# Kernel optimization log

Hardware: AMD Instinct MI355X
Metric: run time of the kernel (lower is better)

Reference implementation:

```python
import jax, jax.numpy as jnp
import numpy as np

SCALING = 2.0  # lora_alpha / r


def setup_inputs() -> dict:
    key = jax.random.key(0)
    ks = jax.random.split(key, 6)
    B, S, D_IN, D_OUT, R = 4, 4096, 4096, 4096, 32
    x = jax.random.normal(ks[0], (B, S, D_IN), dtype=jnp.float32)
    W = jax.random.normal(ks[1], (D_OUT, D_IN), dtype=jnp.float32) * 0.02
    b = jax.random.normal(ks[2], (D_OUT,), dtype=jnp.float32) * 0.02
    A = jax.random.normal(ks[3], (R, D_IN), dtype=jnp.float32) * 0.02
    B_w = jax.random.normal(ks[4], (D_OUT, R), dtype=jnp.float32) * 0.02
    # per-sample activation offsets, in [1, S]
    alora_offsets = jax.random.randint(ks[5], (B,), 1, S + 1, dtype=jnp.int32)
    return {"x": x, "alora_offsets": alora_offsets, "W": W, "b": b, "A": A, "B_w": B_w}


def reference(x, alora_offsets, W, b, A, B_w):
    # base linear: y = x @ W^T + b
    base = jnp.einsum("bsd,od->bso", x, W) + b  # [B, S, D_OUT]
    # LoRA path on full sequence (dropout is identity at inference, p=0)
    lora = jnp.einsum("bsr,or->bso", jnp.einsum("bsd,rd->bsr", x, A), B_w) * SCALING
    # per-sample tail mask: only last k = min(offset, S) positions get the LoRA update
    S = x.shape[1]
    k = jnp.minimum(alora_offsets, S)  # [B]
    pos = jnp.arange(S, dtype=jnp.int32)
    mask = pos[None, :] >= (S - k)[:, None]  # [B, S] True on the tail
    return base + jnp.where(mask[:, :, None], lora, jnp.zeros((), base.dtype))
```

## Files before the change

kernel.cpp:

```cpp
#include <hip/hip_runtime.h>
#include <hip/hip_bf16.h>

typedef __attribute__((ext_vector_type(8))) short short8;
typedef __attribute__((ext_vector_type(4))) float f32x4;

#define GLOAD_LDS16(gp, lp)                                                      \
  __builtin_amdgcn_global_load_lds(                                              \
      (const __attribute__((address_space(1))) void*)(gp),                       \
      (__attribute__((address_space(3))) void*)(lp), 16, 0, 0)

#define SBAR() asm volatile("s_barrier" ::: "memory")
#define VMC(n)                                                                   \
  do {                                                                           \
    asm volatile("s_waitcnt vmcnt(" #n ")" ::: "memory");                        \
    __builtin_amdgcn_sched_barrier(0);                                           \
  } while (0)

__device__ __forceinline__ unsigned short f2bf_rne(float f) {
  union { float f; unsigned int u; } v; v.f = f;
  unsigned int u = v.u;
  u += 0x7fffu + ((u >> 16) & 1u);
  return (unsigned short)(u >> 16);
}

__global__ void cvt_f32_bf16(const float* __restrict__ src,
                             unsigned short* __restrict__ dst, int n8) {
  int i = blockIdx.x * blockDim.x + threadIdx.x;
  int stride = gridDim.x * blockDim.x;
  const f32x4* s4 = (const f32x4*)src;
  short8* d8 = (short8*)dst;
  for (; i < n8; i += stride) {
    f32x4 a = s4[2 * i], b = s4[2 * i + 1];
    short8 o;
    o[0] = (short)f2bf_rne(a[0]); o[1] = (short)f2bf_rne(a[1]);
    o[2] = (short)f2bf_rne(a[2]); o[3] = (short)f2bf_rne(a[3]);
    o[4] = (short)f2bf_rne(b[0]); o[5] = (short)f2bf_rne(b[1]);
    o[6] = (short)f2bf_rne(b[2]); o[7] = (short)f2bf_rne(b[3]);
    d8[i] = o;
  }
}

__global__ __launch_bounds__(256) void lora_t_kernel(
    const unsigned short* __restrict__ xb,
    const unsigned short* __restrict__ Ab,
    const int* __restrict__ offs,
    unsigned short* __restrict__ T)
{
  __shared__ unsigned short xs[64 * 64];
  __shared__ unsigned short as_[32 * 64];
  const int t = threadIdx.x;
  const int m0 = blockIdx.x * 64;
  const int l = t & 63, w = t >> 6;
  const int lr = l & 15, lk = (l >> 4) * 8;
  const int arow = t >> 3, acol = (t & 7) * 8;
  f32x4 acc0 = {0, 0, 0, 0}, acc1 = {0, 0, 0, 0};
  for (int kt = 0; kt < 64; ++kt) {
    __syncthreads();
    const int kof = kt * 64 + acol;
    GLOAD_LDS16(xb + (size_t)(m0 + arow) * 4096 + kof,      (char*)xs + (arow * 64 + acol) * 2);
    GLOAD_LDS16(xb + (size_t)(m0 + 32 + arow) * 4096 + kof, (char*)xs + ((32 + arow) * 64 + acol) * 2);
    GLOAD_LDS16(Ab + (size_t)arow * 4096 + kof,             (char*)as_ + (arow * 64 + acol) * 2);
    __syncthreads();
#pragma unroll
    for (int kk = 0; kk < 2; ++kk) {
      short8 a  = *(const short8*)&xs[(w * 16 + lr) * 64 + kk * 32 + lk];
      short8 b0 = *(const short8*)&as_[lr * 64 + kk * 32 + lk];
      short8 b1 = *(const short8*)&as_[(16 + lr) * 64 + kk * 32 + lk];
      acc0 = __builtin_amdgcn_mfma_f32_16x16x32_bf16(a, b0, acc0, 0, 0, 0);
      acc1 = __builtin_amdgcn_mfma_f32_16x16x32_bf16(a, b1, acc1, 0, 0, 0);
    }
  }
  const int rowb = (l >> 4) * 4;
#pragma unroll
  for (int j = 0; j < 4; ++j) {
    int m = m0 + w * 16 + rowb + j;
    int bb = m >> 12, s = m & 4095;
    int kcut = offs[bb]; if (kcut > 4096) kcut = 4096;
    bool keep = s >= 4096 - kcut;
    T[(size_t)m * 32 + lr]      = keep ? f2bf_rne(2.0f * acc0[j]) : (unsigned short)0;
    T[(size_t)m * 32 + 16 + lr] = keep ? f2bf_rne(2.0f * acc1[j]) : (unsigned short)0;
  }
}

__global__ __launch_bounds__(512, 2) void gemm_kernel(
    const unsigned short* __restrict__ xb,
    const unsigned short* __restrict__ Wb,
    const unsigned short* __restrict__ Tm,
    const unsigned short* __restrict__ Bwb,
    const float* __restrict__ bias,
    float* __restrict__ out)
{
  constexpr int K = 4096;
  extern __shared__ char smem[];

  const int bid = blockIdx.x;
  const int swz = (bid & 7) * 128 + (bid >> 3);
  const int m0 = (swz >> 4) * 256;
  const int n0 = (swz & 15) * 256;

  const int t = threadIdx.x;
  const int l = t & 63, w = t >> 6;
  const int wqr = w >> 2;
  const int pr = (w >> 1) & 1;
  const int pc = w & 1;
  const int lr = l & 15, hi = l >> 4;
  const int e0 = (hi ^ (lr & 7)) * 8;

  const int srow = t >> 3;
  const int schunk = ((t & 7) ^ ((t >> 3) & 7)) * 8;
  const unsigned short* pA0 = xb + (size_t)(m0 + srow) * K + schunk;
  const unsigned short* pA1 = xb + (size_t)(m0 + 128 + srow) * K + schunk;
  const unsigned short* pB0 = Wb + (size_t)(n0 + srow) * K + schunk;
  const unsigned short* pB1 = Wb + (size_t)(n0 + 128 + srow) * K + schunk;
  unsigned short* sm = (unsigned short*)smem;
  const int ldst = t * 16;

#define STG(PTR, SLOT, ISB, HALF, KT)                                           \
  do {                                                                          \
    const unsigned short* g_ = (PTR) + (KT) * 64;                               \
    char* d_ = smem + (SLOT) * 65536 + (ISB) * 32768 + (HALF) * 16384 + ldst;   \
    GLOAD_LDS16(g_, d_);                                                        \
    GLOAD_LDS16(g_ + (size_t)64 * K, d_ + 8192);                                \
  } while (0)

  f32x4 acc[2][4][4];
  short8 afr[4];

  {
    const unsigned short* tp = Tm + (size_t)(m0 + wqr * 128 + pr * 64 + lr) * 32 + hi * 8;
    short8 la[4];
#pragma unroll
    for (int i = 0; i < 4; ++i) la[i] = *(const short8*)(tp + i * 512);
    short8 lb[2][4];
#pragma unroll
    for (int qc = 0; qc < 2; ++qc)
#pragma unroll
      for (int j = 0; j < 4; ++j)
        lb[qc][j] = *(const short8*)(Bwb + (size_t)(n0 + qc * 128 + pc * 64 + j * 16 + lr) * 32 + hi * 8);
#pragma unroll
    for (int qc = 0; qc < 2; ++qc)
#pragma unroll
      for (int i = 0; i < 4; ++i)
#pragma unroll
        for (int j = 0; j < 4; ++j)
          acc[qc][i][j] = __builtin_amdgcn_mfma_f32_16x16x32_bf16(
              la[i], lb[qc][j], (f32x4){0.f, 0.f, 0.f, 0.f}, 0, 0, 0);
  }

  STG(pA0, 0, 0, 0, 0);
  STG(pA1, 0, 0, 1, 0);
  STG(pB0, 0, 1, 0, 0);
  STG(pB1, 0, 1, 1, 0);
  STG(pB0, 1, 1, 0, 1);
  VMC(2);
  SBAR();

#define PHASE(SLOT, QC, KK, READA, STG_STMT, WAIT_STMT)                         \
  {                                                                             \
    const unsigned short* Ah = sm + (SLOT) * 32768 + wqr * 8192;                \
    const unsigned short* Bh = sm + (SLOT) * 32768 + 16384 + (QC) * 8192;       \
    const int ek = e0 ^ ((KK) * 32);                                            \
    if (READA) {                                                                \
      _Pragma("unroll")                                                         \
      for (int i = 0; i < 4; ++i)                                               \
        afr[i] = *(const short8*)(Ah + (pr * 64 + i * 16 + lr) * 64 + ek);      \
    }                                                                           \
    short8 bfr[4];                                                              \
    _Pragma("unroll")                                                           \
    for (int j = 0; j < 4; ++j)                                                 \
      bfr[j] = *(const short8*)(Bh + (pc * 64 + j * 16 + lr) * 64 + ek);        \
    STG_STMT;                                                                   \
    SBAR();                                                                     \
    __builtin_amdgcn_s_setprio(1);                                              \
    _Pragma("unroll")                                                           \
    for (int i = 0; i < 4; ++i)                                                 \
      _Pragma("unroll")                                                         \
      for (int j = 0; j < 4; ++j)                                               \
        acc[QC][i][j] = __builtin_amdgcn_mfma_f32_16x16x32_bf16(                \
            afr[i], bfr[j], acc[QC][i][j], 0, 0, 0);                            \
    __builtin_amdgcn_s_setprio(0);                                              \
    WAIT_STMT;                                                                  \
    SBAR();                                                                     \
  }

  for (int I = 0; I < 31; ++I) {
    const int a = 2 * I;
    PHASE(0, 0, 0, 1, STG(pA0, 1, 0, 0, a + 1), VMC(4));
    PHASE(0, 1, 0, 0, STG(pA1, 1, 0, 1, a + 1), VMC(4));
    PHASE(0, 0, 1, 1, STG(pB1, 1, 1, 1, a + 1), VMC(4));
    PHASE(0, 1, 1, 0, STG(pB0, 0, 1, 0, a + 2), VMC(4));
    PHASE(1, 0, 0, 1, STG(pA0, 0, 0, 0, a + 2), VMC(4));
    PHASE(1, 1, 0, 0, STG(pA1, 0, 0, 1, a + 2), VMC(4));
    PHASE(1, 0, 1, 1, STG(pB1, 0, 1, 1, a + 2), VMC(4));
    PHASE(1, 1, 1, 0, STG(pB0, 1, 1, 0, a + 3), VMC(4));
  }
  PHASE(0, 0, 0, 1, STG(pA0, 1, 0, 0, 63), VMC(4));
  PHASE(0, 1, 0, 0, STG(pA1, 1, 0, 1, 63), VMC(4));
  PHASE(0, 0, 1, 1, STG(pB1, 1, 1, 1, 63), VMC(4));
  PHASE(0, 1, 1, 0, ((void)0), VMC(2));
  PHASE(1, 0, 0, 1, ((void)0), VMC(0));
  PHASE(1, 1, 0, 0, ((void)0), ((void)0));
  PHASE(1, 0, 1, 1, ((void)0), ((void)0));
  PHASE(1, 1, 1, 0, ((void)0), ((void)0));
#undef PHASE
#undef STG

  float bv[2][4];
#pragma unroll
  for (int qc = 0; qc < 2; ++qc)
#pragma unroll
    for (int j = 0; j < 4; ++j)
      bv[qc][j] = bias[n0 + qc * 128 + pc * 64 + j * 16 + lr];
  const int rowb = hi * 4;
#pragma unroll
  for (int qc = 0; qc < 2; ++qc)
#pragma unroll
    for (int i = 0; i < 4; ++i)
#pragma unroll
      for (int e = 0; e < 4; ++e) {
        int row = m0 + wqr * 128 + pr * 64 + i * 16 + rowb + e;
        float* orow = out + (size_t)row * 4096 + n0 + qc * 128 + pc * 64;
#pragma unroll
        for (int j = 0; j < 4; ++j) orow[j * 16 + lr] = acc[qc][i][j][e] + bv[qc][j];
      }
}

extern "C" void kernel_launch(void* const* d_in, const int* in_sizes, int n_in,
                              void* d_out, int out_size, void* d_ws, size_t ws_size,
                              hipStream_t stream) {
  const float* x   = (const float*)d_in[0];
  const int* offs  = (const int*)d_in[1];
  const float* W   = (const float*)d_in[2];
  const float* b   = (const float*)d_in[3];
  const float* A   = (const float*)d_in[4];
  const float* Bw  = (const float*)d_in[5];
  float* out = (float*)d_out;

  char* ws = (char*)d_ws;
  unsigned short* xb  = (unsigned short*)ws;
  unsigned short* Wb  = (unsigned short*)(ws + 134217728);
  unsigned short* Ab  = (unsigned short*)(ws + 167772160);
  unsigned short* Bwb = (unsigned short*)(ws + 168034304);
  unsigned short* T   = (unsigned short*)(ws + 168296448);

  hipFuncSetAttribute((const void*)gemm_kernel,
                      hipFuncAttributeMaxDynamicSharedMemorySize, 131072);

  cvt_f32_bf16<<<2048, 256, 0, stream>>>(x, xb, 67108864 / 8);
  cvt_f32_bf16<<<2048, 256, 0, stream>>>(W, Wb, 16777216 / 8);
  cvt_f32_bf16<<<64, 256, 0, stream>>>(A, Ab, 131072 / 8);
  cvt_f32_bf16<<<64, 256, 0, stream>>>(Bw, Bwb, 131072 / 8);
  lora_t_kernel<<<256, 256, 0, stream>>>(xb, Ab, offs, T);
  gemm_kernel<<<1024, 512, 131072, stream>>>(xb, Wb, T, Bwb, b, out);
}
```

Baseline: 604.4 us.

## Restructure main GEMM loop into windows with early-issued LDS fragment reads

Replaces the per-phase macro with a four-phase window that preloads A and B fragments for upcoming phases ahead of the barriers. The MFMA order is reshuffled (qc0/kk0, qc1/kk0, qc0/kk1, qc1/kk1) so LDS reads for the next phase can overlap the current MFMA block. The vmcnt waits in the last phase of each window are relaxed. This uses more fragment registers, which may raise VGPR pressure, and the changed wait counts must still cover the LDS slot reuse hazards.

Result: no change. 608.4 us (+0.7%).

```diff
diff --git a/kernel.cpp b/kernel.cpp
--- a/kernel.cpp
+++ b/kernel.cpp
@@ -124,7 +124,25 @@
   } while (0)
 
   f32x4 acc[2][4][4];
-  short8 afr[4];
+  short8 a0f[4], a1f[4], b0f[4], b1f[4];
+
+#define RD_A(DST, AH, KK)                                                       \
+  _Pragma("unroll")                                                             \
+  for (int i_ = 0; i_ < 4; ++i_)                                                \
+    DST[i_] = *(const short8*)((AH) + (pr * 64 + i_ * 16 + lr) * 64 + (e0 ^ ((KK) * 32)));
+
+#define RD_B(DST, BH, KK)                                                       \
+  _Pragma("unroll")                                                             \
+  for (int j_ = 0; j_ < 4; ++j_)                                                \
+    DST[j_] = *(const short8*)((BH) + (pc * 64 + j_ * 16 + lr) * 64 + (e0 ^ ((KK) * 32)));
+
+#define MFMA16(QC, AF, BF)                                                      \
+  _Pragma("unroll")                                                             \
+  for (int i_ = 0; i_ < 4; ++i_)                                                \
+    _Pragma("unroll")                                                           \
+    for (int j_ = 0; j_ < 4; ++j_)                                              \
+      acc[QC][i_][j_] = __builtin_amdgcn_mfma_f32_16x16x32_bf16(                \
+          (AF)[i_], (BF)[j_], acc[QC][i_][j_], 0, 0, 0);
 
   {
     const unsigned short* tp = Tm + (size_t)(m0 + wqr * 128 + pr * 64 + lr) * 32 + hi * 8;
@@ -155,54 +173,51 @@
   VMC(2);
   SBAR();
 
-#define PHASE(SLOT, QC, KK, READA, STG_STMT, WAIT_STMT)                         \
+#define WINDOW(SLOT, S0, S1, S2, S3, W0, W1, W2, W3)                            \
   {                                                                             \
-    const unsigned short* Ah = sm + (SLOT) * 32768 + wqr * 8192;                \
-    const unsigned short* Bh = sm + (SLOT) * 32768 + 16384 + (QC) * 8192;       \
-    const int ek = e0 ^ ((KK) * 32);                                            \
-    if (READA) {                                                                \
-      _Pragma("unroll")                                                         \
-      for (int i = 0; i < 4; ++i)                                               \
-        afr[i] = *(const short8*)(Ah + (pr * 64 + i * 16 + lr) * 64 + ek);      \
-    }                                                                           \
-    short8 bfr[4];                                                              \
-    _Pragma("unroll")                                                           \
-    for (int j = 0; j < 4; ++j)                                                 \
-      bfr[j] = *(const short8*)(Bh + (pc * 64 + j * 16 + lr) * 64 + ek);        \
-    STG_STMT;                                                                   \
-    SBAR();                                                                     \
-    __builtin_amdgcn_s_setprio(1);                                              \
-    _Pragma("unroll")                                                           \
-    for (int i = 0; i < 4; ++i)                                                 \
-      _Pragma("unroll")                                                         \
-      for (int j = 0; j < 4; ++j)                                               \
-        acc[QC][i][j] = __builtin_amdgcn_mfma_f32_16x16x32_bf16(                \
-            afr[i], bfr[j], acc[QC][i][j], 0, 0, 0);                            \
-    __builtin_amdgcn_s_setprio(0);                                              \
-    WAIT_STMT;                                                                  \
-    SBAR();                                                                     \
+    const unsigned short* Ah  = sm + (SLOT) * 32768 + wqr * 8192;               \
+    const unsigned short* B0h = sm + (SLOT) * 32768 + 16384;                    \
+    const unsigned short* B1h = sm + (SLOT) * 32768 + 16384 + 8192;             \
+    RD_A(a0f, Ah, 0); RD_B(b0f, B0h, 0);                \
+                                                             \
+    RD_B(b1f, B1h, 0);                                                          \
+    S0; SBAR();                                                                 \
+    __builtin_amdgcn_s_setprio(1); MFMA16(0, a0f, b0f);                         \
+    __builtin_amdgcn_s_setprio(0); W0; SBAR();                                  \
+                                                             \
+    RD_A(a1f, Ah, 1); RD_B(b0f, B0h, 1);                                        \
+    S1; SBAR();                                                                 \
+    __builtin_amdgcn_s_setprio(1); MFMA16(1, a0f, b1f);                         \
+    __builtin_amdgcn_s_setprio(0); W1; SBAR();                                  \
+                                                             \
+    RD_B(b1f, B1h, 1);                                                          \
+    S2; SBAR();                                                                 \
+    __builtin_amdgcn_s_setprio(1); MFMA16(0, a1f, b0f);                         \
+    __builtin_amdgcn_s_setprio(0); W2; SBAR();                                  \
+                                                             \
+    S3; SBAR();                                                                 \
+    __builtin_amdgcn_s_setprio(1); MFMA16(1, a1f, b1f);                         \
+    __builtin_amdgcn_s_setprio(0); W3; SBAR();                                  \
   }
 
   for (int I = 0; I < 31; ++I) {
     const int a = 2 * I;
-    PHASE(0, 0, 0, 1, STG(pA0, 1, 0, 0, a + 1), VMC(4));
-    PHASE(0, 1, 0, 0, STG(pA1, 1, 0, 1, a + 1), VMC(4));
-    PHASE(0, 0, 1, 1, STG(pB1, 1, 1, 1, a + 1), VMC(4));
-    PHASE(0, 1, 1, 0, STG(pB0, 0, 1, 0, a + 2), VMC(4));
-    PHASE(1, 0, 0, 1, STG(pA0, 0, 0, 0, a + 2), VMC(4));
-    PHASE(1, 1, 0, 0, STG(pA1, 0, 0, 1, a + 2), VMC(4));
-    PHASE(1, 0, 1, 1, STG(pB1, 0, 1, 1, a + 2), VMC(4));
-    PHASE(1, 1, 1, 0, STG(pB0, 1, 1, 0, a + 3), VMC(4));
-  }
-  PHASE(0, 0, 0, 1, STG(pA0, 1, 0, 0, 63), VMC(4));
-  PHASE(0, 1, 0, 0, STG(pA1, 1, 0, 1, 63), VMC(4));
-  PHASE(0, 0, 1, 1, STG(pB1, 1, 1, 1, 63), VMC(4));
-  PHASE(0, 1, 1, 0, ((void)0), VMC(2));
-  PHASE(1, 0, 0, 1, ((void)0), VMC(0));
-  PHASE(1, 1, 0, 0, ((void)0), ((void)0));
-  PHASE(1, 0, 1, 1, ((void)0), ((void)0));
-  PHASE(1, 1, 1, 0, ((void)0), ((void)0));
-#undef PHASE
+    WINDOW(0, STG(pA0, 1, 0, 0, a + 1), STG(pA1, 1, 0, 1, a + 1),
+              STG(pB1, 1, 1, 1, a + 1), STG(pB0, 0, 1, 0, a + 2),
+              VMC(4), VMC(4), VMC(4), VMC(2));
+    WINDOW(1, STG(pA0, 0, 0, 0, a + 2), STG(pA1, 0, 0, 1, a + 2),
+              STG(pB1, 0, 1, 1, a + 2), STG(pB0, 1, 1, 0, a + 3),
+              VMC(4), VMC(4), VMC(4), VMC(2));
+  }
+  WINDOW(0, STG(pA0, 1, 0, 0, 63), STG(pA1, 1, 0, 1, 63),
+            STG(pB1, 1, 1, 1, 63), ((void)0),
+            VMC(4), VMC(4), VMC(2), VMC(0));
+  WINDOW(1, ((void)0), ((void)0), ((void)0), ((void)0),
+            ((void)0), ((void)0), ((void)0), ((void)0));
+#undef WINDOW
+#undef MFMA16
+#undef RD_A
+#undef RD_B
 #undef STG
 
   float bv[2][4];
```

## Switch main GEMM to 32x32x16 MFMA with reworked LDS pipeline schedule

Applied to the files above, without the earlier changes.

Replaces the 16x16x32 bf16 MFMA tiling with 32x32x16 MFMA, so each wave computes 2x2x2 tiles of 32x32 and uses fewer LDS reads per FLOP. The pipeline is restructured too: each K-slot now has four k-sub-phases that each load full A and B fragments, staging is grouped as whole-A and whole-B double-buffer loads, and waits are a full vmcnt(0) once per slot instead of fine-grained vmcnt(4). The LoRA init and epilogue are adapted to the 32x32 accumulator layout. The coarser waits may expose more load latency.

New measurement: 662.7 us. +9.6%, slower.

```diff
diff --git a/kernel.cpp b/kernel.cpp
--- a/kernel.cpp
+++ b/kernel.cpp
@@ -3,6 +3,7 @@
 
 typedef __attribute__((ext_vector_type(8))) short short8;
 typedef __attribute__((ext_vector_type(4))) float f32x4;
+typedef __attribute__((ext_vector_type(16))) float f32x16;
 
 #define GLOAD_LDS16(gp, lp)                                                      \
   __builtin_amdgcn_global_load_lds(                                              \
@@ -103,8 +104,8 @@
   const int wqr = w >> 2;
   const int pr = (w >> 1) & 1;
   const int pc = w & 1;
-  const int lr = l & 15, hi = l >> 4;
-  const int e0 = (hi ^ (lr & 7)) * 8;
+  const int la = l & 31, ksel = l >> 5;
+  const int cxor = la & 7;
 
   const int srow = t >> 3;
   const int schunk = ((t & 7) ^ ((t >> 3) & 7)) * 8;
@@ -122,107 +123,110 @@
     GLOAD_LDS16(g_, d_);                                                        \
     GLOAD_LDS16(g_ + (size_t)64 * K, d_ + 8192);                                \
   } while (0)
-
-  f32x4 acc[2][4][4];
-  short8 afr[4];
+#define STGA(SLOT, KT) do { STG(pA0, SLOT, 0, 0, KT); STG(pA1, SLOT, 0, 1, KT); } while (0)
+#define STGB(SLOT, KT) do { STG(pB0, SLOT, 1, 0, KT); STG(pB1, SLOT, 1, 1, KT); } while (0)
+
+  const int rowbase = m0 + wqr * 128 + pr * 64;
+  const int arowbase = (wqr * 128 + pr * 64) * 64;
+
+  f32x16 acc[2][2][2];
 
   {
-    const unsigned short* tp = Tm + (size_t)(m0 + wqr * 128 + pr * 64 + lr) * 32 + hi * 8;
-    short8 la[4];
-#pragma unroll
-    for (int i = 0; i < 4; ++i) la[i] = *(const short8*)(tp + i * 512);
-    short8 lb[2][4];
+    short8 ta[2][2];
+#pragma unroll
+    for (int i = 0; i < 2; ++i)
+#pragma unroll
+      for (int ks = 0; ks < 2; ++ks)
+        ta[i][ks] = *(const short8*)(Tm + (size_t)(rowbase + i * 32 + la) * 32 + ks * 16 + ksel * 8);
+    const f32x16 z16 = {0.f, 0.f, 0.f, 0.f, 0.f, 0.f, 0.f, 0.f,
+                        0.f, 0.f, 0.f, 0.f, 0.f, 0.f, 0.f, 0.f};
 #pragma unroll
     for (int qc = 0; qc < 2; ++qc)
 #pragma unroll
-      for (int j = 0; j < 4; ++j)
-        lb[qc][j] = *(const short8*)(Bwb + (size_t)(n0 + qc * 128 + pc * 64 + j * 16 + lr) * 32 + hi * 8);
-#pragma unroll
-    for (int qc = 0; qc < 2; ++qc)
-#pragma unroll
-      for (int i = 0; i < 4; ++i)
-#pragma unroll
-        for (int j = 0; j < 4; ++j)
-          acc[qc][i][j] = __builtin_amdgcn_mfma_f32_16x16x32_bf16(
-              la[i], lb[qc][j], (f32x4){0.f, 0.f, 0.f, 0.f}, 0, 0, 0);
-  }
-
-  STG(pA0, 0, 0, 0, 0);
-  STG(pA1, 0, 0, 1, 0);
-  STG(pB0, 0, 1, 0, 0);
-  STG(pB1, 0, 1, 1, 0);
-  STG(pB0, 1, 1, 0, 1);
-  VMC(2);
+      for (int j = 0; j < 2; ++j) {
+        const unsigned short* bp = Bwb + (size_t)(n0 + qc * 128 + pc * 64 + j * 32 + la) * 32;
+        short8 tb0 = *(const short8*)(bp + ksel * 8);
+        short8 tb1 = *(const short8*)(bp + 16 + ksel * 8);
+#pragma unroll
+        for (int i = 0; i < 2; ++i) {
+          f32x16 v = __builtin_amdgcn_mfma_f32_32x32x16_bf16(ta[i][0], tb0, z16, 0, 0, 0);
+          acc[qc][i][j] = __builtin_amdgcn_mfma_f32_32x32x16_bf16(ta[i][1], tb1, v, 0, 0, 0);
+        }
+      }
+  }
+
+  STGA(0, 0); STGB(0, 0);
+  VMC(0);
   SBAR();
 
-#define PHASE(SLOT, QC, KK, READA, STG_STMT, WAIT_STMT)                         \
+#define PHASE(SLOT, KS, WAIT, ...)                                              \
   {                                                                             \
-    const unsigned short* Ah = sm + (SLOT) * 32768 + wqr * 8192;                \
-    const unsigned short* Bh = sm + (SLOT) * 32768 + 16384 + (QC) * 8192;       \
-    const int ek = e0 ^ ((KK) * 32);                                            \
-    if (READA) {                                                                \
+    const unsigned short* Sb = sm + (SLOT) * 32768;                             \
+    const int ck = ((((KS) * 2) + ksel) ^ cxor) * 8;                            \
+    short8 afr[2], bfr[2][2];                                                   \
+    _Pragma("unroll")                                                           \
+    for (int i_ = 0; i_ < 2; ++i_)                                              \
+      afr[i_] = *(const short8*)(Sb + arowbase + (i_ * 32 + la) * 64 + ck);     \
+    _Pragma("unroll")                                                           \
+    for (int q_ = 0; q_ < 2; ++q_)                                              \
       _Pragma("unroll")                                                         \
-      for (int i = 0; i < 4; ++i)                                               \
-        afr[i] = *(const short8*)(Ah + (pr * 64 + i * 16 + lr) * 64 + ek);      \
-    }                                                                           \
-    short8 bfr[4];                                                              \
-    _Pragma("unroll")                                                           \
-    for (int j = 0; j < 4; ++j)                                                 \
-      bfr[j] = *(const short8*)(Bh + (pc * 64 + j * 16 + lr) * 64 + ek);        \
-    STG_STMT;                                                                   \
+      for (int j_ = 0; j_ < 2; ++j_)                                            \
+        bfr[q_][j_] = *(const short8*)(Sb + 16384 +                             \
+            (q_ * 128 + pc * 64 + j_ * 32 + la) * 64 + ck);                     \
+    __VA_ARGS__;                                                                \
     SBAR();                                                                     \
     __builtin_amdgcn_s_setprio(1);                                              \
     _Pragma("unroll")                                                           \
-    for (int i = 0; i < 4; ++i)                                                 \
+    for (int q_ = 0; q_ < 2; ++q_)                                              \
       _Pragma("unroll")                                                         \
-      for (int j = 0; j < 4; ++j)                                               \
-        acc[QC][i][j] = __builtin_amdgcn_mfma_f32_16x16x32_bf16(                \
-            afr[i], bfr[j], acc[QC][i][j], 0, 0, 0);                            \
+      for (int i_ = 0; i_ < 2; ++i_)                                            \
+        _Pragma("unroll")                                                       \
+        for (int j_ = 0; j_ < 2; ++j_)                                          \
+          acc[q_][i_][j_] = __builtin_amdgcn_mfma_f32_32x32x16_bf16(            \
+              afr[i_], bfr[q_][j_], acc[q_][i_][j_], 0, 0, 0);                  \
     __builtin_amdgcn_s_setprio(0);                                              \
-    WAIT_STMT;                                                                  \
+    WAIT;                                                                       \
     SBAR();                                                                     \
   }
 
   for (int I = 0; I < 31; ++I) {
     const int a = 2 * I;
-    PHASE(0, 0, 0, 1, STG(pA0, 1, 0, 0, a + 1), VMC(4));
-    PHASE(0, 1, 0, 0, STG(pA1, 1, 0, 1, a + 1), VMC(4));
-    PHASE(0, 0, 1, 1, STG(pB1, 1, 1, 1, a + 1), VMC(4));
-    PHASE(0, 1, 1, 0, STG(pB0, 0, 1, 0, a + 2), VMC(4));
-    PHASE(1, 0, 0, 1, STG(pA0, 0, 0, 0, a + 2), VMC(4));
-    PHASE(1, 1, 0, 0, STG(pA1, 0, 0, 1, a + 2), VMC(4));
-    PHASE(1, 0, 1, 1, STG(pB1, 0, 1, 1, a + 2), VMC(4));
-    PHASE(1, 1, 1, 0, STG(pB0, 1, 1, 0, a + 3), VMC(4));
-  }
-  PHASE(0, 0, 0, 1, STG(pA0, 1, 0, 0, 63), VMC(4));
-  PHASE(0, 1, 0, 0, STG(pA1, 1, 0, 1, 63), VMC(4));
-  PHASE(0, 0, 1, 1, STG(pB1, 1, 1, 1, 63), VMC(4));
-  PHASE(0, 1, 1, 0, ((void)0), VMC(2));
-  PHASE(1, 0, 0, 1, ((void)0), VMC(0));
-  PHASE(1, 1, 0, 0, ((void)0), ((void)0));
-  PHASE(1, 0, 1, 1, ((void)0), ((void)0));
-  PHASE(1, 1, 1, 0, ((void)0), ((void)0));
+    PHASE(0, 0, ((void)0), STGA(1, a + 1));
+    PHASE(0, 1, ((void)0), STGB(1, a + 1));
+    PHASE(0, 2, ((void)0), );
+    PHASE(0, 3, VMC(0), );
+    PHASE(1, 0, ((void)0), STGA(0, a + 2));
+    PHASE(1, 1, ((void)0), STGB(0, a + 2));
+    PHASE(1, 2, ((void)0), );
+    PHASE(1, 3, VMC(0), );
+  }
+  PHASE(0, 0, ((void)0), STGA(1, 63));
+  PHASE(0, 1, ((void)0), STGB(1, 63));
+  PHASE(0, 2, ((void)0), );
+  PHASE(0, 3, VMC(0), );
+  PHASE(1, 0, ((void)0), );
+  PHASE(1, 1, ((void)0), );
+  PHASE(1, 2, ((void)0), );
+  PHASE(1, 3, ((void)0), );
 #undef PHASE
+#undef STGA
+#undef STGB
 #undef STG
 
-  float bv[2][4];
 #pragma unroll
   for (int qc = 0; qc < 2; ++qc)
 #pragma unroll
-    for (int j = 0; j < 4; ++j)
-      bv[qc][j] = bias[n0 + qc * 128 + pc * 64 + j * 16 + lr];
-  const int rowb = hi * 4;
-#pragma unroll
-  for (int qc = 0; qc < 2; ++qc)
-#pragma unroll
-    for (int i = 0; i < 4; ++i)
-#pragma unroll
-      for (int e = 0; e < 4; ++e) {
-        int row = m0 + wqr * 128 + pr * 64 + i * 16 + rowb + e;
-        float* orow = out + (size_t)row * 4096 + n0 + qc * 128 + pc * 64;
-#pragma unroll
-        for (int j = 0; j < 4; ++j) orow[j * 16 + lr] = acc[qc][i][j][e] + bv[qc][j];
-      }
+    for (int j = 0; j < 2; ++j) {
+      const int cb = n0 + qc * 128 + pc * 64 + j * 32;
+      const float bvv = bias[cb + la];
+#pragma unroll
+      for (int i = 0; i < 2; ++i)
+#pragma unroll
+        for (int r = 0; r < 16; ++r) {
+          const int row = rowbase + i * 32 + (r & 3) + 8 * (r >> 2) + 4 * ksel;
+          out[(size_t)row * 4096 + cb + la] = acc[qc][i][j][r] + bvv;
+        }
+    }
 }
 
 extern "C" void kernel_launch(void* const* d_in, const int* in_sizes, int n_in,
```

## Shrink GEMM tile to 128x128 with 256 threads and simpler double buffering

Applied to the files above, without the earlier changes.

Changes the main GEMM from 256x256 tiles with 8 waves to 128x128 tiles with 4 waves, launching 4096 blocks with 64KB of LDS. The fine-grained 8-phase staggered pipeline is replaced by a two-slot double buffer that prefetches the next K tile and does a full vmcnt(0) wait each K step. This lowers per-block register and LDS use and raises the block count. In exchange, arithmetic intensity per tile is lower, so more global traffic goes to x and W, and the full wait weakens load overlap.

Result: slower. 768.2 us (+27.1%).

```diff
diff --git a/kernel.cpp b/kernel.cpp
--- a/kernel.cpp
+++ b/kernel.cpp
@@ -82,7 +82,7 @@
   }
 }
 
-__global__ __launch_bounds__(512, 2) void gemm_kernel(
+__global__ __launch_bounds__(256, 2) void gemm_kernel(
     const unsigned short* __restrict__ xb,
     const unsigned short* __restrict__ Wb,
     const unsigned short* __restrict__ Tm,
@@ -94,90 +94,81 @@
   extern __shared__ char smem[];
 
   const int bid = blockIdx.x;
-  const int swz = (bid & 7) * 128 + (bid >> 3);
-  const int m0 = (swz >> 4) * 256;
-  const int n0 = (swz & 15) * 256;
+  const int swz = (bid & 7) * 512 + (bid >> 3);
+  const int m0 = (swz >> 5) * 128;
+  const int n0 = (swz & 31) * 128;
 
   const int t = threadIdx.x;
   const int l = t & 63, w = t >> 6;
-  const int wqr = w >> 2;
-  const int pr = (w >> 1) & 1;
-  const int pc = w & 1;
+  const int wr = w >> 1, wc = w & 1;
   const int lr = l & 15, hi = l >> 4;
   const int e0 = (hi ^ (lr & 7)) * 8;
 
   const int srow = t >> 3;
   const int schunk = ((t & 7) ^ ((t >> 3) & 7)) * 8;
-  const unsigned short* pA0 = xb + (size_t)(m0 + srow) * K + schunk;
-  const unsigned short* pA1 = xb + (size_t)(m0 + 128 + srow) * K + schunk;
-  const unsigned short* pB0 = Wb + (size_t)(n0 + srow) * K + schunk;
-  const unsigned short* pB1 = Wb + (size_t)(n0 + 128 + srow) * K + schunk;
+  const unsigned short* pAg = xb + (size_t)(m0 + srow) * K + schunk;
+  const unsigned short* pBg = Wb + (size_t)(n0 + srow) * K + schunk;
   unsigned short* sm = (unsigned short*)smem;
   const int ldst = t * 16;
 
-#define STG(PTR, SLOT, ISB, HALF, KT)                                           \
+#define STGA(SLOT, KT)                                                          \
   do {                                                                          \
-    const unsigned short* g_ = (PTR) + (KT) * 64;                               \
-    char* d_ = smem + (SLOT) * 65536 + (ISB) * 32768 + (HALF) * 16384 + ldst;   \
-    GLOAD_LDS16(g_, d_);                                                        \
-    GLOAD_LDS16(g_ + (size_t)64 * K, d_ + 8192);                                \
+    _Pragma("unroll")                                                           \
+    for (int q_ = 0; q_ < 4; ++q_)                                              \
+      GLOAD_LDS16(pAg + (size_t)q_ * 32 * K + (KT) * 64,                        \
+                  smem + (SLOT) * 32768 + q_ * 4096 + ldst);                    \
   } while (0)
-
-  f32x4 acc[2][4][4];
-  short8 afr[4];
+#define STGB(SLOT, KT)                                                          \
+  do {                                                                          \
+    _Pragma("unroll")                                                           \
+    for (int q_ = 0; q_ < 4; ++q_)                                              \
+      GLOAD_LDS16(pBg + (size_t)q_ * 32 * K + (KT) * 64,                        \
+                  smem + (SLOT) * 32768 + 16384 + q_ * 4096 + ldst);            \
+  } while (0)
+
+  f32x4 acc[4][4];
 
   {
-    const unsigned short* tp = Tm + (size_t)(m0 + wqr * 128 + pr * 64 + lr) * 32 + hi * 8;
-    short8 la[4];
-#pragma unroll
-    for (int i = 0; i < 4; ++i) la[i] = *(const short8*)(tp + i * 512);
-    short8 lb[2][4];
-#pragma unroll
-    for (int qc = 0; qc < 2; ++qc)
+    short8 la[4], lb[4];
+#pragma unroll
+    for (int i = 0; i < 4; ++i)
+      la[i] = *(const short8*)(Tm + (size_t)(m0 + wr * 64 + i * 16 + lr) * 32 + hi * 8);
+#pragma unroll
+    for (int j = 0; j < 4; ++j)
+      lb[j] = *(const short8*)(Bwb + (size_t)(n0 + wc * 64 + j * 16 + lr) * 32 + hi * 8);
+#pragma unroll
+    for (int i = 0; i < 4; ++i)
 #pragma unroll
       for (int j = 0; j < 4; ++j)
-        lb[qc][j] = *(const short8*)(Bwb + (size_t)(n0 + qc * 128 + pc * 64 + j * 16 + lr) * 32 + hi * 8);
-#pragma unroll
-    for (int qc = 0; qc < 2; ++qc)
-#pragma unroll
-      for (int i = 0; i < 4; ++i)
-#pragma unroll
-        for (int j = 0; j < 4; ++j)
-          acc[qc][i][j] = __builtin_amdgcn_mfma_f32_16x16x32_bf16(
-              la[i], lb[qc][j], (f32x4){0.f, 0.f, 0.f, 0.f}, 0, 0, 0);
-  }
-
-  STG(pA0, 0, 0, 0, 0);
-  STG(pA1, 0, 0, 1, 0);
-  STG(pB0, 0, 1, 0, 0);
-  STG(pB1, 0, 1, 1, 0);
-  STG(pB0, 1, 1, 0, 1);
-  VMC(2);
+        acc[i][j] = __builtin_amdgcn_mfma_f32_16x16x32_bf16(
+            la[i], lb[j], (f32x4){0.f, 0.f, 0.f, 0.f}, 0, 0, 0);
+  }
+
+  STGA(0, 0); STGB(0, 0);
+  VMC(0);
   SBAR();
 
-#define PHASE(SLOT, QC, KK, READA, STG_STMT, WAIT_STMT)                         \
+#define PHASE(SLOT, KK, STG_STMT, WAIT_STMT)                                    \
   {                                                                             \
-    const unsigned short* Ah = sm + (SLOT) * 32768 + wqr * 8192;                \
-    const unsigned short* Bh = sm + (SLOT) * 32768 + 16384 + (QC) * 8192;       \
+    const unsigned short* As = sm + (SLOT) * 16384;                             \
+    const unsigned short* Bs = sm + (SLOT) * 16384 + 8192;                      \
     const int ek = e0 ^ ((KK) * 32);                                            \
-    if (READA) {                                                                \
-      _Pragma("unroll")                                                         \
-      for (int i = 0; i < 4; ++i)                                               \
-        afr[i] = *(const short8*)(Ah + (pr * 64 + i * 16 + lr) * 64 + ek);      \
-    }                                                                           \
-    short8 bfr[4];                                                              \
-    _Pragma("unroll")                                                           \
-    for (int j = 0; j < 4; ++j)                                                 \
-      bfr[j] = *(const short8*)(Bh + (pc * 64 + j * 16 + lr) * 64 + ek);        \
+    short8 af[4], bf[4];                                                        \
+    _Pragma("unroll")                                                           \
+    for (int i_ = 0; i_ < 4; ++i_)                                              \
+      af[i_] = *(const short8*)(As + (wr * 64 + i_ * 16 + lr) * 64 + ek);       \
+    _Pragma("unroll")                                                           \
+    for (int j_ = 0; j_ < 4; ++j_)                                              \
+      bf[j_] = *(const short8*)(Bs + (wc * 64 + j_ * 16 + lr) * 64 + ek);       \
     STG_STMT;                                                                   \
     SBAR();                                                                     \
     __builtin_amdgcn_s_setprio(1);                                              \
     _Pragma("unroll")                                                           \
-    for (int i = 0; i < 4; ++i)                                                 \
+    for (int i_ = 0; i_ < 4; ++i_)                                              \
       _Pragma("unroll")                                                         \
-      for (int j = 0; j < 4; ++j)                                               \
-        acc[QC][i][j] = __builtin_amdgcn_mfma_f32_16x16x32_bf16(                \
-            afr[i], bfr[j], acc[QC][i][j], 0, 0, 0);                            \
+      for (int j_ = 0; j_ < 4; ++j_)                                            \
+        acc[i_][j_] = __builtin_amdgcn_mfma_f32_16x16x32_bf16(                  \
+            af[i_], bf[j_], acc[i_][j_], 0, 0, 0);                              \
     __builtin_amdgcn_s_setprio(0);                                              \
     WAIT_STMT;                                                                  \
     SBAR();                                                                     \
@@ -185,44 +176,32 @@
 
   for (int I = 0; I < 31; ++I) {
     const int a = 2 * I;
-    PHASE(0, 0, 0, 1, STG(pA0, 1, 0, 0, a + 1), VMC(4));
-    PHASE(0, 1, 0, 0, STG(pA1, 1, 0, 1, a + 1), VMC(4));
-    PHASE(0, 0, 1, 1, STG(pB1, 1, 1, 1, a + 1), VMC(4));
-    PHASE(0, 1, 1, 0, STG(pB0, 0, 1, 0, a + 2), VMC(4));
-    PHASE(1, 0, 0, 1, STG(pA0, 0, 0, 0, a + 2), VMC(4));
-    PHASE(1, 1, 0, 0, STG(pA1, 0, 0, 1, a + 2), VMC(4));
-    PHASE(1, 0, 1, 1, STG(pB1, 0, 1, 1, a + 2), VMC(4));
-    PHASE(1, 1, 1, 0, STG(pB0, 1, 1, 0, a + 3), VMC(4));
-  }
-  PHASE(0, 0, 0, 1, STG(pA0, 1, 0, 0, 63), VMC(4));
-  PHASE(0, 1, 0, 0, STG(pA1, 1, 0, 1, 63), VMC(4));
-  PHASE(0, 0, 1, 1, STG(pB1, 1, 1, 1, 63), VMC(4));
-  PHASE(0, 1, 1, 0, ((void)0), VMC(2));
-  PHASE(1, 0, 0, 1, ((void)0), VMC(0));
-  PHASE(1, 1, 0, 0, ((void)0), ((void)0));
-  PHASE(1, 0, 1, 1, ((void)0), ((void)0));
-  PHASE(1, 1, 1, 0, ((void)0), ((void)0));
+    PHASE(0, 0, { STGA(1, a + 1); STGB(1, a + 1); }, ((void)0));
+    PHASE(0, 1, ((void)0), VMC(0));
+    PHASE(1, 0, { STGA(0, a + 2); STGB(0, a + 2); }, ((void)0));
+    PHASE(1, 1, ((void)0), VMC(0));
+  }
+  PHASE(0, 0, { STGA(1, 63); STGB(1, 63); }, ((void)0));
+  PHASE(0, 1, ((void)0), VMC(0));
+  PHASE(1, 0, ((void)0), ((void)0));
+  PHASE(1, 1, ((void)0), ((void)0));
 #undef PHASE
-#undef STG
-
-  float bv[2][4];
-#pragma unroll
-  for (int qc = 0; qc < 2; ++qc)
-#pragma unroll
-    for (int j = 0; j < 4; ++j)
-      bv[qc][j] = bias[n0 + qc * 128 + pc * 64 + j * 16 + lr];
+#undef STGA
+#undef STGB
+
+  float bv[4];
+#pragma unroll
+  for (int j = 0; j < 4; ++j) bv[j] = bias[n0 + wc * 64 + j * 16 + lr];
   const int rowb = hi * 4;
 #pragma unroll
-  for (int qc = 0; qc < 2; ++qc)
-#pragma unroll
-    for (int i = 0; i < 4; ++i)
-#pragma unroll
-      for (int e = 0; e < 4; ++e) {
-        int row = m0 + wqr * 128 + pr * 64 + i * 16 + rowb + e;
-        float* orow = out + (size_t)row * 4096 + n0 + qc * 128 + pc * 64;
-#pragma unroll
-        for (int j = 0; j < 4; ++j) orow[j * 16 + lr] = acc[qc][i][j][e] + bv[qc][j];
-      }
+  for (int i = 0; i < 4; ++i)
+#pragma unroll
+    for (int e = 0; e < 4; ++e) {
+      int row = m0 + wr * 64 + i * 16 + rowb + e;
+      float* orow = out + (size_t)row * 4096 + n0 + wc * 64;
+#pragma unroll
+      for (int j = 0; j < 4; ++j) orow[j * 16 + lr] = acc[i][j][e] + bv[j];
+    }
 }
 
 extern "C" void kernel_launch(void* const* d_in, const int* in_sizes, int n_in,
@@ -244,12 +223,12 @@
   unsigned short* T   = (unsigned short*)(ws + 168296448);
 
   hipFuncSetAttribute((const void*)gemm_kernel,
-                      hipFuncAttributeMaxDynamicSharedMemorySize, 131072);
+                      hipFuncAttributeMaxDynamicSharedMemorySize, 65536);
 
   cvt_f32_bf16<<<2048, 256, 0, stream>>>(x, xb, 67108864 / 8);
   cvt_f32_bf16<<<2048, 256, 0, stream>>>(W, Wb, 16777216 / 8);
   cvt_f32_bf16<<<64, 256, 0, stream>>>(A, Ab, 131072 / 8);
   cvt_f32_bf16<<<64, 256, 0, stream>>>(Bw, Bwb, 131072 / 8);
   lora_t_kernel<<<256, 256, 0, stream>>>(xb, Ab, offs, T);
-  gemm_kernel<<<1024, 512, 131072, stream>>>(xb, Wb, T, Bwb, b, out);
-}
+  gemm_kernel<<<4096, 256, 65536, stream>>>(xb, Wb, T, Bwb, b, out);
+}
```
